# Performance work log

Hardware: AMD Instinct MI355X
Metric: run time of the kernel (lower is better)

The kernel has to match this reference:

```python
import jax, jax.numpy as jnp
import numpy as np

DIM = 512
NUM_HEADS = 8
HEAD_DIM = DIM // NUM_HEADS
MAX_SLICES = 1024
SCALE = float(np.sqrt(HEAD_DIM))


def setup_inputs() -> dict:
    key = jax.random.key(0)
    ks = jax.random.split(key, 12)
    B, Nv, Nt, D = 4, 1024, 512, DIM
    std = 0.02
    inp = {
        "visual_tokens": jax.random.normal(ks[0], (B, Nv, D), jnp.float32),
        "text_tokens": jax.random.normal(ks[1], (B, Nt, D), jnp.float32),
        # Linear weights stored as [in, out] (i.e., torch W^T), so y = x @ W + b
        "W_Q": jax.random.normal(ks[2], (D, D), jnp.float32) * std,
        "b_Q": jnp.zeros((D,), jnp.float32),
        "W_K": jax.random.normal(ks[3], (D, D), jnp.float32) * std,
        "b_K": jnp.zeros((D,), jnp.float32),
        "W_V": jax.random.normal(ks[4], (D, D), jnp.float32) * std,
        "b_V": jnp.zeros((D,), jnp.float32),
        "W_O": jax.random.normal(ks[5], (D, D), jnp.float32) * std,
        "b_O": jnp.zeros((D,), jnp.float32),
        "bias_table": jax.random.normal(ks[6], (2 * MAX_SLICES - 1, NUM_HEADS), jnp.float32) * std,
        "ln_gamma": jnp.ones((D,), jnp.float32),
        "ln_beta": jnp.zeros((D,), jnp.float32),
    }
    return inp


def _layernorm(x, gamma, beta, eps=1e-5):
    mu = jnp.mean(x, axis=-1, keepdims=True)
    var = jnp.var(x, axis=-1, keepdims=True)
    return (x - mu) * jax.lax.rsqrt(var + eps) * gamma + beta


def reference(visual_tokens, text_tokens, W_Q, b_Q, W_K, b_K, W_V, b_V, W_O, b_O,
              bias_table, ln_gamma, ln_beta):
    Z = jnp.concatenate([visual_tokens, text_tokens], axis=1)  # [B, N, D]
    B, N, D = Z.shape
    Z = _layernorm(Z, ln_gamma, ln_beta)

    def proj(W, b):
        return (Z @ W + b).reshape(B, N, NUM_HEADS, HEAD_DIM).transpose(0, 2, 1, 3)

    Q = proj(W_Q, b_Q)  # [B, H, N, hd]
    K = proj(W_K, b_K)
    V = proj(W_V, b_V)

    attn = jnp.einsum("bhqd,bhkd->bhqk", Q, K) / SCALE  # [B, H, N, N]

    # relative slice bias: [H, N, N]
    coords = jnp.arange(N)
    rel = coords[:, None] - coords[None, :] + (MAX_SLICES - 1)
    rel = jnp.clip(rel, 0, 2 * MAX_SLICES - 2)
    bias = bias_table[rel]                      # [N, N, H]
    bias = jnp.transpose(bias, (2, 0, 1))[None]  # [1, H, N, N]

    attn = jax.nn.softmax(attn + bias, axis=-1)
    out = jnp.einsum("bhqk,bhkd->bhqd", attn, V)  # [B, H, N, hd]
    out = out.transpose(0, 2, 1, 3).reshape(B, N, D)
    return out @ W_O + b_O
```

## Files before the change

kernel.cpp:

```cpp
#include <hip/hip_runtime.h>
#include <stdint.h>

#define NSEQ   1536
#define NBATCH 4
#define NM     (NBATCH * NSEQ)
#define DMODEL 512
#define NHEAD  8
#define HD     64
#define TBLN   2047

typedef __attribute__((ext_vector_type(4)))  float f32x4;
typedef __attribute__((ext_vector_type(16))) float f32x16;
typedef __attribute__((ext_vector_type(4)))  int   i32x4;
typedef __attribute__((ext_vector_type(2)))  unsigned u32x2;
typedef __attribute__((ext_vector_type(8)))  __bf16 bf16x8;
typedef unsigned short u16;

static_assert(sizeof(bf16x8) == 16, "bf16x8 must be 16B");

__device__ inline u16 f2bf(float f) {
  union { float f; uint32_t u; } v; v.f = f;
  uint32_t u = v.u;
  return (u16)((u + 0x7fffu + ((u >> 16) & 1u)) >> 16);
}

__device__ inline bf16x8 ld_bf8(const u16* p) {
  i32x4 v = *(const i32x4*)p;
  return __builtin_bit_cast(bf16x8, v);
}

__device__ inline f32x4 mfma16(bf16x8 a, bf16x8 b, f32x4 c) {
  return __builtin_amdgcn_mfma_f32_16x16x32_bf16(a, b, c, 0, 0, 0);
}

__device__ inline f32x16 mfma32(bf16x8 a, bf16x8 b, f32x16 c) {
  return __builtin_amdgcn_mfma_f32_32x32x16_bf16(a, b, c, 0, 0, 0);
}

__device__ inline void gload_lds16(const void* g, void* l) {
  __builtin_amdgcn_global_load_lds(
      (__attribute__((address_space(1))) void*)(g),
      (__attribute__((address_space(3))) void*)(l), 16, 0, 0);
}

__device__ inline uint32_t pkbf(float a, float b) {
  uint32_t r;
  asm("v_cvt_pk_bf16_f32 %0, %1, %2" : "=v"(r) : "v"(a), "v"(b));
  return r;
}

__device__ inline void plswap(uint32_t& a, uint32_t& b, int hi) {
#if __has_builtin(__builtin_amdgcn_permlane32_swap)
  u32x2 r = __builtin_amdgcn_permlane32_swap(a, b, false, false);
  a = r[0]; b = r[1];
#else
  const uint32_t as = (uint32_t)__shfl_xor((int)a, 32);
  const uint32_t bs = (uint32_t)__shfl_xor((int)b, 32);
  const uint32_t na = hi ? bs : a;
  const uint32_t nb = hi ? b : as;
  a = na; b = nb;
#endif
}

__device__ inline float exp2_raw(float x) {
  float r;
  asm("v_exp_f32 %0, %1" : "=v"(r) : "v"(x));
  return r;
}

__device__ inline float bfhi(uint32_t u) {
  union { uint32_t u; float f; } v; v.u = u & 0xffff0000u; return v.f;
}
__device__ inline float bflo(uint32_t u) {
  union { uint32_t u; float f; } v; v.u = u << 16; return v.f;
}

__global__ __launch_bounds__(256) void ln_kernel(
    const float* __restrict__ vis, const float* __restrict__ txt,
    const float* __restrict__ gamma, const float* __restrict__ beta,
    u16* __restrict__ zn) {
  const int lane = threadIdx.x & 63;
  const int row  = blockIdx.x * 4 + (threadIdx.x >> 6);
  const int b = row / NSEQ, n = row - b * NSEQ;
  const float* src = (n < 1024) ? (vis + ((size_t)b * 1024 + n) * DMODEL)
                                : (txt + ((size_t)b * 512 + (n - 1024)) * DMODEL);
  const float4* s4 = (const float4*)src;
  float4 x0 = s4[lane], x1 = s4[lane + 64];
  float s = x0.x + x0.y + x0.z + x0.w + x1.x + x1.y + x1.z + x1.w;
  float q = x0.x*x0.x + x0.y*x0.y + x0.z*x0.z + x0.w*x0.w
          + x1.x*x1.x + x1.y*x1.y + x1.z*x1.z + x1.w*x1.w;
  #pragma unroll
  for (int m = 1; m < 64; m <<= 1) { s += __shfl_xor(s, m); q += __shfl_xor(q, m); }
  const float mean = s * (1.0f / 512.0f);
  const float var  = q * (1.0f / 512.0f) - mean * mean;
  const float rstd = rsqrtf(var + 1e-5f);
  const float4* g4 = (const float4*)gamma;
  const float4* b4 = (const float4*)beta;
  float4 g0 = g4[lane], g1 = g4[lane + 64], p0 = b4[lane], p1 = b4[lane + 64];
  u16* dst = zn + (size_t)row * DMODEL;
  ushort4 o0, o1;
  o0.x = f2bf((x0.x - mean) * rstd * g0.x + p0.x);
  o0.y = f2bf((x0.y - mean) * rstd * g0.y + p0.y);
  o0.z = f2bf((x0.z - mean) * rstd * g0.z + p0.z);
  o0.w = f2bf((x0.w - mean) * rstd * g0.w + p0.w);
  o1.x = f2bf((x1.x - mean) * rstd * g1.x + p1.x);
  o1.y = f2bf((x1.y - mean) * rstd * g1.y + p1.y);
  o1.z = f2bf((x1.z - mean) * rstd * g1.z + p1.z);
  o1.w = f2bf((x1.w - mean) * rstd * g1.w + p1.w);
  *(ushort4*)(dst + lane * 4)        = o0;
  *(ushort4*)(dst + (lane + 64) * 4) = o1;
}

__global__ __launch_bounds__(256) void wtrans_kernel(
    const float* __restrict__ WQ, const float* __restrict__ WK,
    const float* __restrict__ WV, const float* __restrict__ WO,
    u16* __restrict__ wqkvt, u16* __restrict__ wot) {
  __shared__ float t[32][33];
  const int m = blockIdx.z;
  const float* W = (m == 0) ? WQ : (m == 1) ? WK : (m == 2) ? WV : WO;
  const int n0 = blockIdx.x * 32, k0 = blockIdx.y * 32;
  const int tx = threadIdx.x & 31, ty = threadIdx.x >> 5;
  #pragma unroll
  for (int j = 0; j < 4; ++j)
    t[ty + j * 8][tx] = W[(size_t)(k0 + ty + j * 8) * DMODEL + n0 + tx];
  __syncthreads();
  u16* out = (m < 3) ? (wqkvt + (size_t)m * DMODEL * DMODEL) : wot;
  #pragma unroll
  for (int j = 0; j < 4; ++j)
    out[(size_t)(n0 + ty + j * 8) * DMODEL + k0 + tx] = f2bf(t[tx][ty + j * 8]);
}

__global__ __launch_bounds__(256, 2) void gemm_qkv(
    const u16* __restrict__ A, const u16* __restrict__ Bt,
    const float* __restrict__ bQ, const float* __restrict__ bK, const float* __restrict__ bV,
    u16* __restrict__ Q, u16* __restrict__ Kk, u16* __restrict__ Vt) {
  __shared__ __align__(16) u16 lat[2][192 * 64];
  __shared__ __align__(16) u16 lbt[2][96 * 64];
  const int tid = threadIdx.x, lane = tid & 63, w = tid >> 6;
  const int wr = w >> 1, wc = w & 1;
  const int m0 = blockIdx.y * 192, n0 = blockIdx.x * 96;
  f32x4 acc[6][3] = {};
#define QSTAGE(buf, k0)                                                        \
  do {                                                                         \
    _Pragma("unroll")                                                          \
    for (int i = 0; i < 6; ++i) {                                              \
      int ch = tid + 256 * i;                              \
      int row = ch >> 3, pc = ch & 7;                                          \
      int kk = (k0) + ((pc ^ (row & 7)) << 3);                                 \
      gload_lds16(A + (size_t)(m0 + row) * DMODEL + kk, lat[buf] + (size_t)ch * 8); \
    }                                                                          \
    _Pragma("unroll")                                                          \
    for (int i = 0; i < 3; ++i) {                                              \
      int ch = tid + 256 * i;                               \
      int row = ch >> 3, pc = ch & 7;                                          \
      int kk = (k0) + ((pc ^ (row & 7)) << 3);                                 \
      gload_lds16(Bt + (size_t)(n0 + row) * DMODEL + kk, lbt[buf] + (size_t)ch * 8); \
    }                                                                          \
  } while (0)

  QSTAGE(0, 0);
  __syncthreads();
  int cur = 0;
  for (int kt = 0; kt < 8; ++kt) {
    const int nxt = cur ^ 1;
    if (kt < 7) {
      QSTAGE(nxt, (kt + 1) * 64);
      asm volatile("s_waitcnt vmcnt(9)" ::: "memory");
    } else {
      asm volatile("s_waitcnt vmcnt(0)" ::: "memory");
    }
    __builtin_amdgcn_s_barrier();
    #pragma unroll
    for (int ks = 0; ks < 2; ++ks) {
      bf16x8 af[6], bfr[3];
      const int cc = ks * 4 + (lane >> 4);
      #pragma unroll
      for (int f = 0; f < 6; ++f) {
        int ra = wr * 96 + f * 16 + (lane & 15);
        af[f]  = ld_bf8(lat[cur] + ra * 64 + ((cc ^ (ra & 7)) << 3));
      }
      #pragma unroll
      for (int f = 0; f < 3; ++f) {
        int rb = wc * 48 + f * 16 + (lane & 15);
        bfr[f] = ld_bf8(lbt[cur] + rb * 64 + ((cc ^ (rb & 7)) << 3));
      }
      __builtin_amdgcn_s_setprio(1);
      #pragma unroll
      for (int fr = 0; fr < 6; ++fr)
        #pragma unroll
        for (int fc = 0; fc < 3; ++fc)
          acc[fr][fc] = mfma16(af[fr], bfr[fc], acc[fr][fc]);
      __builtin_amdgcn_s_setprio(0);
    }
    __builtin_amdgcn_s_barrier();
    cur = nxt;
  }
  #pragma unroll
  for (int fr = 0; fr < 6; ++fr) {
    const int mbase = m0 + wr * 96 + fr * 16 + ((lane >> 4) << 2);
    const int b = mbase / NSEQ;
    const int nseq = mbase - b * NSEQ;
    #pragma unroll
    for (int fc = 0; fc < 3; ++fc) {
      const int col = n0 + wc * 48 + fc * 16 + (lane & 15);
      const int which = col >> 9;
      const int cw = col & 511;
      const int h = cw >> 6, d = cw & 63;
      const float bias = (which == 0) ? bQ[cw] : (which == 1) ? bK[cw] : bV[cw];
      if (which < 2) {
        u16* dst = ((which == 0) ? Q : Kk) + ((size_t)(b * NHEAD + h) * NSEQ + nseq) * HD + d;
        #pragma unroll
        for (int r = 0; r < 4; ++r) dst[(size_t)r * HD] = f2bf(acc[fr][fc][r] + bias);
      } else {
        ushort4 pv;
        pv.x = f2bf(acc[fr][fc][0] + bias);
        pv.y = f2bf(acc[fr][fc][1] + bias);
        pv.z = f2bf(acc[fr][fc][2] + bias);
        pv.w = f2bf(acc[fr][fc][3] + bias);
        *(ushort4*)(Vt + ((size_t)(b * NHEAD + h) * HD + d) * NSEQ + nseq) = pv;
      }
    }
  }
#undef QSTAGE
}

__global__ __launch_bounds__(256, 2) void gemm_oproj(
    const u16* __restrict__ A, const u16* __restrict__ Bt,
    const float* __restrict__ bO, float* __restrict__ out) {
  __shared__ __align__(16) u16 lat[2][96 * 64];
  __shared__ __align__(16) u16 lbt[2][64 * 64];
  const int tid = threadIdx.x, lane = tid & 63, w = tid >> 6;
  const int wr = w >> 1, wc = w & 1;
  const int m0 = blockIdx.y * 96, n0 = blockIdx.x * 64;
  f32x4 acc[3][2] = {};
#define OSTAGE(buf, k0)                                                        \
  do {                                                                         \
    _Pragma("unroll")                                                          \
    for (int i = 0; i < 3; ++i) {                                              \
      int ch = tid + 256 * i;                               \
      int row = ch >> 3, pc = ch & 7;                                          \
      int kk = (k0) + ((pc ^ (row & 7)) << 3);                                 \
      gload_lds16(A + (size_t)(m0 + row) * DMODEL + kk, lat[buf] + (size_t)ch * 8); \
    }                                                                          \
    _Pragma("unroll")                                                          \
    for (int i = 0; i < 2; ++i) {                                              \
      int ch = tid + 256 * i;                               \
      int row = ch >> 3, pc = ch & 7;                                          \
      int kk = (k0) + ((pc ^ (row & 7)) << 3);                                 \
      gload_lds16(Bt + (size_t)(n0 + row) * DMODEL + kk, lbt[buf] + (size_t)ch * 8); \
    }                                                                          \
  } while (0)

  OSTAGE(0, 0);
  __syncthreads();
  int cur = 0;
  for (int kt = 0; kt < 8; ++kt) {
    const int nxt = cur ^ 1;
    if (kt < 7) {
      OSTAGE(nxt, (kt + 1) * 64);
      asm volatile("s_waitcnt vmcnt(5)" ::: "memory");
    } else {
      asm volatile("s_waitcnt vmcnt(0)" ::: "memory");
    }
    __builtin_amdgcn_s_barrier();
    #pragma unroll
    for (int ks = 0; ks < 2; ++ks) {
      bf16x8 af[3], bfr[2];
      const int cc = ks * 4 + (lane >> 4);
      #pragma unroll
      for (int f = 0; f < 3; ++f) {
        int ra = wr * 48 + f * 16 + (lane & 15);
        af[f]  = ld_bf8(lat[cur] + ra * 64 + ((cc ^ (ra & 7)) << 3));
      }
      #pragma unroll
      for (int f = 0; f < 2; ++f) {
        int rb = wc * 32 + f * 16 + (lane & 15);
        bfr[f] = ld_bf8(lbt[cur] + rb * 64 + ((cc ^ (rb & 7)) << 3));
      }
      __builtin_amdgcn_s_setprio(1);
      #pragma unroll
      for (int fr = 0; fr < 3; ++fr)
        #pragma unroll
        for (int fc = 0; fc < 2; ++fc)
          acc[fr][fc] = mfma16(af[fr], bfr[fc], acc[fr][fc]);
      __builtin_amdgcn_s_setprio(0);
    }
    __builtin_amdgcn_s_barrier();
    cur = nxt;
  }
  #pragma unroll
  for (int fr = 0; fr < 3; ++fr) {
    const int mbase = m0 + wr * 48 + fr * 16 + ((lane >> 4) << 2);
    #pragma unroll
    for (int fc = 0; fc < 2; ++fc) {
      const int col = n0 + wc * 32 + fc * 16 + (lane & 15);
      const float bias = bO[col];
      float* dst = out + (size_t)mbase * DMODEL + col;
      #pragma unroll
      for (int r = 0; r < 4; ++r) dst[(size_t)r * DMODEL] = acc[fr][fc][r] + bias;
    }
  }
#undef OSTAGE
}

__global__ __launch_bounds__(768, 3) void attn_kernel(
    const u16* __restrict__ Q, const u16* __restrict__ K,
    const u16* __restrict__ Vt, const float* __restrict__ table,
    u16* __restrict__ O) {
  __shared__ __align__(16) char smem[77824];
  u16* rb2k = (u16*)smem;
  const int tid = threadIdx.x, lane = tid & 63, w = tid >> 6;
  const int bid = blockIdx.x;
  const int xcd = bid & 7, idx = bid >> 3;
  const int bh  = xcd * 4 + (idx & 3);
  const int qt  = idx >> 2;
  const int h   = bh & (NHEAD - 1);
  for (int t = tid; t < 2 * 3072; t += 768) {
    const int c = (t >= 3072) ? 1 : 0;
    const int x = t - c * 3072;
    int src = 2558 - (x + c);
    src = src < 0 ? 0 : (src > 2046 ? 2046 : src);
    rb2k[c * 3072 + x] = f2bf(table[(size_t)src * NHEAD + h] * 1.4426950408889634f);
  }

  const int lo32 = lane & 31, hi = lane >> 5;
  const int ws = (w < 6) ? w : (w - 6);
  const int hf = (w < 6) ? 0 : 1;
  const int kbase = hf * 768;
  const int q  = qt * 192 + ws * 32 + lo32;
  const u16* Qb = Q  + (size_t)bh * NSEQ * HD;
  const u16* Kb = K  + (size_t)bh * NSEQ * HD;
  const u16* Vb = Vt + (size_t)bh * HD * NSEQ;

  const int tloc = tid - hf * 384;
  u16* kl0 = (u16*)(smem + 12288) + hf * 2 * 4096;
  u16* vl0 = (u16*)(smem + 45056) + hf * 2 * 4096;
#define STAGE(b, k0loc)                                                       \
  if (tloc < 256) {                                                           \
    _Pragma("unroll")                                                         \
    for (int i = 0; i < 2; ++i) {                                             \
      int ch = tloc + 256 * i;                                                \
      int row = ch >> 3, pc = ch & 7;                                         \
      int col = (pc ^ (row & 7)) << 3;                                        \
      gload_lds16(Kb + (size_t)(kbase + (k0loc) + row) * HD + col,            \
                  kl0 + (size_t)(b) * 4096 + ch * 8);                         \
      gload_lds16(Vb + (size_t)row * NSEQ + kbase + (k0loc) + col,            \
                  vl0 + (size_t)(b) * 4096 + ch * 8);                         \
    }                                                                         \
  }

  bf16x8 qf[4];
  #pragma unroll
  for (int ds = 0; ds < 4; ++ds)
    qf[ds] = ld_bf8(Qb + (size_t)q * HD + ds * 16 + hi * 8);

  float l_part = 0.f;
  f32x16 acc[2] = {};

  const int rswz = lo32 & 7;
  const int T0  = 1535 - q + 4 * hi + kbase;
  const int c2  = T0 & 1;
  const int dwb = (T0 - c2) >> 1;
  const uint32_t* rbp32 = (const uint32_t*)(rb2k + c2 * 3072);
  const float c1 = 0.125f * 1.4426950408889634f;

  STAGE(0, 0);
  __syncthreads();
  int cur = 0;

  for (int kt = 0; kt < 12; ++kt) {
    const int nxt = cur ^ 1;
    if (kt < 11) {
      STAGE(nxt, (kt + 1) * 64);
      asm volatile("s_waitcnt vmcnt(4)" ::: "memory");
    } else {
      asm volatile("s_waitcnt vmcnt(0)" ::: "memory");
    }
    __builtin_amdgcn_s_barrier();
    const u16* kb = (u16*)(smem + 12288) + (hf * 2 + cur) * 4096;
    const u16* vb = (u16*)(smem + 45056) + (hf * 2 + cur) * 4096;
    #pragma unroll
    for (int ktile = 0; ktile < 2; ++ktile) {
      f32x16 st = {};
      __builtin_amdgcn_s_setprio(1);
      #pragma unroll
      for (int ds = 0; ds < 4; ++ds) {
        const int row = ktile * 32 + lo32;
        const bf16x8 kf = ld_bf8(kb + row * 64 + (((2 * ds + hi) ^ rswz) << 3));
        st = mfma32(kf, qf[ds], st);
      }
      __builtin_amdgcn_s_setprio(0);
      const int dwk = dwb + ((kt * 64 + ktile * 32) >> 1);
      float bv[4][4];
      #pragma unroll
      for (int gp = 0; gp < 4; ++gp) {
        const uint32_t u0 = rbp32[dwk + 4 * gp];
        const uint32_t u1 = rbp32[dwk + 4 * gp + 1];
        bv[gp][0] = bflo(u0); bv[gp][1] = bfhi(u0);
        bv[gp][2] = bflo(u1); bv[gp][3] = bfhi(u1);
      }
      #pragma unroll
      for (int r = 0; r < 16; ++r) {
        float p = exp2_raw(__builtin_fmaf(st[r], c1, bv[r >> 2][r & 3]));
        st[r] = p;
        l_part += p;
      }
      uint32_t wv[8];
      #pragma unroll
      for (int i = 0; i < 8; ++i) wv[i] = pkbf(st[2 * i], st[2 * i + 1]);
      plswap(wv[0], wv[2], hi);  plswap(wv[1], wv[3], hi);
      plswap(wv[4], wv[6], hi);  plswap(wv[5], wv[7], hi);
      i32x4 b0; b0[0] = (int)wv[0]; b0[1] = (int)wv[1]; b0[2] = (int)wv[2]; b0[3] = (int)wv[3];
      i32x4 b1; b1[0] = (int)wv[4]; b1[1] = (int)wv[5]; b1[2] = (int)wv[6]; b1[3] = (int)wv[7];
      const bf16x8 pb0 = __builtin_bit_cast(bf16x8, b0);
      const bf16x8 pb1 = __builtin_bit_cast(bf16x8, b1);
      __builtin_amdgcn_s_setprio(1);
      #pragma unroll
      for (int dh = 0; dh < 2; ++dh) {
        const int vrow = dh * 32 + lo32;
        const bf16x8 va0 = ld_bf8(vb + vrow * 64 + (((4 * ktile + 0 + hi) ^ rswz) << 3));
        acc[dh] = mfma32(va0, pb0, acc[dh]);
        const bf16x8 va1 = ld_bf8(vb + vrow * 64 + (((4 * ktile + 2 + hi) ^ rswz) << 3));
        acc[dh] = mfma32(va1, pb1, acc[dh]);
      }
      __builtin_amdgcn_s_setprio(0);
    }
    __builtin_amdgcn_s_barrier();
    cur = nxt;
  }
  float* scr = (float*)(smem + 12288);
  if (hf == 1) {
    float* wb = scr + ws * 2112;
    #pragma unroll
    for (int dh = 0; dh < 2; ++dh)
      #pragma unroll
      for (int i = 0; i < 4; ++i) {
        f32x4 c4; c4[0] = acc[dh][4*i]; c4[1] = acc[dh][4*i+1];
        c4[2] = acc[dh][4*i+2]; c4[3] = acc[dh][4*i+3];
        ((f32x4*)wb)[(dh * 4 + i) * 64 + lane] = c4;
      }
    wb[2048 + lane] = l_part;
  }
  __syncthreads();
  if (hf == 0) {
    const float* rb = scr + ws * 2112;
    #pragma unroll
    for (int dh = 0; dh < 2; ++dh)
      #pragma unroll
      for (int i = 0; i < 4; ++i) {
        const f32x4 c4 = ((const f32x4*)rb)[(dh * 4 + i) * 64 + lane];
        acc[dh][4*i] += c4[0]; acc[dh][4*i+1] += c4[1];
        acc[dh][4*i+2] += c4[2]; acc[dh][4*i+3] += c4[3];
      }
    l_part += rb[2048 + lane];
    float l_r = l_part + __shfl_xor(l_part, 32);
    const float inv = 1.0f / l_r;
    const int b = bh >> 3;
    u16* orow = O + ((size_t)(b * NSEQ + q)) * DMODEL + h * HD;
    #pragma unroll
    for (int dh = 0; dh < 2; ++dh)
      #pragma unroll
      for (int gp = 0; gp < 4; ++gp) {
        uint2 o4;
        o4.x = pkbf(acc[dh][4*gp]   * inv, acc[dh][4*gp+1] * inv);
        o4.y = pkbf(acc[dh][4*gp+2] * inv, acc[dh][4*gp+3] * inv);
        *(uint2*)(orow + dh * 32 + 8 * gp + 4 * hi) = o4;
      }
  }
#undef STAGE
}

extern "C" void kernel_launch(void* const* d_in, const int* in_sizes, int n_in,
                              void* d_out, int out_size, void* d_ws, size_t ws_size,
                              hipStream_t stream) {
  const float* vis   = (const float*)d_in[0];
  const float* txt   = (const float*)d_in[1];
  const float* WQ    = (const float*)d_in[2];
  const float* bQ    = (const float*)d_in[3];
  const float* WK    = (const float*)d_in[4];
  const float* bK    = (const float*)d_in[5];
  const float* WV    = (const float*)d_in[6];
  const float* bV    = (const float*)d_in[7];
  const float* WO    = (const float*)d_in[8];
  const float* bO    = (const float*)d_in[9];
  const float* table = (const float*)d_in[10];
  const float* gamma = (const float*)d_in[11];
  const float* beta  = (const float*)d_in[12];
  float* out = (float*)d_out;

  char* p = (char*)d_ws;
  u16* zn    = (u16*)p; p += (size_t)NM * DMODEL * 2;
  u16* wqkvt = (u16*)p; p += (size_t)3 * DMODEL * DMODEL * 2;
  u16* wot   = (u16*)p; p += (size_t)DMODEL * DMODEL * 2;
  u16* q     = (u16*)p; p += (size_t)NM * DMODEL * 2;
  u16* k     = (u16*)p; p += (size_t)NM * DMODEL * 2;
  u16* vt    = (u16*)p; p += (size_t)NM * DMODEL * 2;
  u16* o     = (u16*)p; p += (size_t)NM * DMODEL * 2;

  hipLaunchKernelGGL(ln_kernel, dim3(NM / 4), dim3(256), 0, stream,
                     vis, txt, gamma, beta, zn);
  hipLaunchKernelGGL(wtrans_kernel, dim3(16, 16, 4), dim3(256), 0, stream,
                     WQ, WK, WV, WO, wqkvt, wot);
  hipLaunchKernelGGL(gemm_qkv, dim3(16, 32), dim3(256), 0, stream,
                     zn, wqkvt, bQ, bK, bV, q, k, vt);
  hipLaunchKernelGGL(attn_kernel, dim3(256), dim3(768), 0, stream,
                     q, k, vt, table, o);
  hipLaunchKernelGGL(gemm_oproj, dim3(8, 64), dim3(256), 0, stream,
                     o, wot, bO, out);
}
```

Baseline: 75.44 us.

## Deepen attention K/V staging to 4-buffer ring and fuse prep kernels

The attention kernel now keeps four K/V LDS buffers and prefetches two tiles ahead, which lets it drop the trailing per-iteration barrier. The layernorm and weight-transpose kernels are merged into one launch that dispatches on block index. The aim is to hide global-load latency in attention and save one kernel launch. In exchange, attention LDS use roughly doubles and the vmcnt wait counts may not match the deeper prefetch.

```diff
diff --git a/kernel.cpp b/kernel.cpp
--- a/kernel.cpp
+++ b/kernel.cpp
@@ -75,59 +75,60 @@
   union { uint32_t u; float f; } v; v.u = u << 16; return v.f;
 }
 
-__global__ __launch_bounds__(256) void ln_kernel(
+__global__ __launch_bounds__(256) void prep_kernel(
     const float* __restrict__ vis, const float* __restrict__ txt,
     const float* __restrict__ gamma, const float* __restrict__ beta,
-    u16* __restrict__ zn) {
-  const int lane = threadIdx.x & 63;
-  const int row  = blockIdx.x * 4 + (threadIdx.x >> 6);
-  const int b = row / NSEQ, n = row - b * NSEQ;
-  const float* src = (n < 1024) ? (vis + ((size_t)b * 1024 + n) * DMODEL)
-                                : (txt + ((size_t)b * 512 + (n - 1024)) * DMODEL);
-  const float4* s4 = (const float4*)src;
-  float4 x0 = s4[lane], x1 = s4[lane + 64];
-  float s = x0.x + x0.y + x0.z + x0.w + x1.x + x1.y + x1.z + x1.w;
-  float q = x0.x*x0.x + x0.y*x0.y + x0.z*x0.z + x0.w*x0.w
-          + x1.x*x1.x + x1.y*x1.y + x1.z*x1.z + x1.w*x1.w;
-  #pragma unroll
-  for (int m = 1; m < 64; m <<= 1) { s += __shfl_xor(s, m); q += __shfl_xor(q, m); }
-  const float mean = s * (1.0f / 512.0f);
-  const float var  = q * (1.0f / 512.0f) - mean * mean;
-  const float rstd = rsqrtf(var + 1e-5f);
-  const float4* g4 = (const float4*)gamma;
-  const float4* b4 = (const float4*)beta;
-  float4 g0 = g4[lane], g1 = g4[lane + 64], p0 = b4[lane], p1 = b4[lane + 64];
-  u16* dst = zn + (size_t)row * DMODEL;
-  ushort4 o0, o1;
-  o0.x = f2bf((x0.x - mean) * rstd * g0.x + p0.x);
-  o0.y = f2bf((x0.y - mean) * rstd * g0.y + p0.y);
-  o0.z = f2bf((x0.z - mean) * rstd * g0.z + p0.z);
-  o0.w = f2bf((x0.w - mean) * rstd * g0.w + p0.w);
-  o1.x = f2bf((x1.x - mean) * rstd * g1.x + p1.x);
-  o1.y = f2bf((x1.y - mean) * rstd * g1.y + p1.y);
-  o1.z = f2bf((x1.z - mean) * rstd * g1.z + p1.z);
-  o1.w = f2bf((x1.w - mean) * rstd * g1.w + p1.w);
-  *(ushort4*)(dst + lane * 4)        = o0;
-  *(ushort4*)(dst + (lane + 64) * 4) = o1;
-}
-
-__global__ __launch_bounds__(256) void wtrans_kernel(
     const float* __restrict__ WQ, const float* __restrict__ WK,
     const float* __restrict__ WV, const float* __restrict__ WO,
-    u16* __restrict__ wqkvt, u16* __restrict__ wot) {
+    u16* __restrict__ zn, u16* __restrict__ wqkvt, u16* __restrict__ wot) {
   __shared__ float t[32][33];
-  const int m = blockIdx.z;
-  const float* W = (m == 0) ? WQ : (m == 1) ? WK : (m == 2) ? WV : WO;
-  const int n0 = blockIdx.x * 32, k0 = blockIdx.y * 32;
-  const int tx = threadIdx.x & 31, ty = threadIdx.x >> 5;
-  #pragma unroll
-  for (int j = 0; j < 4; ++j)
-    t[ty + j * 8][tx] = W[(size_t)(k0 + ty + j * 8) * DMODEL + n0 + tx];
-  __syncthreads();
-  u16* out = (m < 3) ? (wqkvt + (size_t)m * DMODEL * DMODEL) : wot;
-  #pragma unroll
-  for (int j = 0; j < 4; ++j)
-    out[(size_t)(n0 + ty + j * 8) * DMODEL + k0 + tx] = f2bf(t[tx][ty + j * 8]);
+  if (blockIdx.x < 1536) {
+    const int lane = threadIdx.x & 63;
+    const int row  = blockIdx.x * 4 + (threadIdx.x >> 6);
+    const int b = row / NSEQ, n = row - b * NSEQ;
+    const float* src = (n < 1024) ? (vis + ((size_t)b * 1024 + n) * DMODEL)
+                                  : (txt + ((size_t)b * 512 + (n - 1024)) * DMODEL);
+    const float4* s4 = (const float4*)src;
+    float4 x0 = s4[lane], x1 = s4[lane + 64];
+    float s = x0.x + x0.y + x0.z + x0.w + x1.x + x1.y + x1.z + x1.w;
+    float q = x0.x*x0.x + x0.y*x0.y + x0.z*x0.z + x0.w*x0.w
+            + x1.x*x1.x + x1.y*x1.y + x1.z*x1.z + x1.w*x1.w;
+    #pragma unroll
+    for (int m = 1; m < 64; m <<= 1) { s += __shfl_xor(s, m); q += __shfl_xor(q, m); }
+    const float mean = s * (1.0f / 512.0f);
+    const float var  = q * (1.0f / 512.0f) - mean * mean;
+    const float rstd = rsqrtf(var + 1e-5f);
+    const float4* g4 = (const float4*)gamma;
+    const float4* b4 = (const float4*)beta;
+    float4 g0 = g4[lane], g1 = g4[lane + 64], p0 = b4[lane], p1 = b4[lane + 64];
+    u16* dst = zn + (size_t)row * DMODEL;
+    ushort4 o0, o1;
+    o0.x = f2bf((x0.x - mean) * rstd * g0.x + p0.x);
+    o0.y = f2bf((x0.y - mean) * rstd * g0.y + p0.y);
+    o0.z = f2bf((x0.z - mean) * rstd * g0.z + p0.z);
+    o0.w = f2bf((x0.w - mean) * rstd * g0.w + p0.w);
+    o1.x = f2bf((x1.x - mean) * rstd * g1.x + p1.x);
+    o1.y = f2bf((x1.y - mean) * rstd * g1.y + p1.y);
+    o1.z = f2bf((x1.z - mean) * rstd * g1.z + p1.z);
+    o1.w = f2bf((x1.w - mean) * rstd * g1.w + p1.w);
+    *(ushort4*)(dst + lane * 4)        = o0;
+    *(ushort4*)(dst + (lane + 64) * 4) = o1;
+  } else {
+    const int id = blockIdx.x - 1536;
+    const int m = id & 3;
+    const int rem = id >> 2;
+    const float* W = (m == 0) ? WQ : (m == 1) ? WK : (m == 2) ? WV : WO;
+    const int n0 = (rem & 15) * 32, k0 = (rem >> 4) * 32;
+    const int tx = threadIdx.x & 31, ty = threadIdx.x >> 5;
+    #pragma unroll
+    for (int j = 0; j < 4; ++j)
+      t[ty + j * 8][tx] = W[(size_t)(k0 + ty + j * 8) * DMODEL + n0 + tx];
+    __syncthreads();
+    u16* out = (m < 3) ? (wqkvt + (size_t)m * DMODEL * DMODEL) : wot;
+    #pragma unroll
+    for (int j = 0; j < 4; ++j)
+      out[(size_t)(n0 + ty + j * 8) * DMODEL + k0 + tx] = f2bf(t[tx][ty + j * 8]);
+  }
 }
 
 __global__ __launch_bounds__(256, 2) void gemm_qkv(
@@ -144,14 +145,14 @@
   do {                                                                         \
     _Pragma("unroll")                                                          \
     for (int i = 0; i < 6; ++i) {                                              \
-      int ch = tid + 256 * i;                              \
+      int ch = tid + 256 * i;                                                  \
       int row = ch >> 3, pc = ch & 7;                                          \
       int kk = (k0) + ((pc ^ (row & 7)) << 3);                                 \
       gload_lds16(A + (size_t)(m0 + row) * DMODEL + kk, lat[buf] + (size_t)ch * 8); \
     }                                                                          \
     _Pragma("unroll")                                                          \
     for (int i = 0; i < 3; ++i) {                                              \
-      int ch = tid + 256 * i;                               \
+      int ch = tid + 256 * i;                                                  \
       int row = ch >> 3, pc = ch & 7;                                          \
       int kk = (k0) + ((pc ^ (row & 7)) << 3);                                 \
       gload_lds16(Bt + (size_t)(n0 + row) * DMODEL + kk, lbt[buf] + (size_t)ch * 8); \
@@ -237,14 +238,14 @@
   do {                                                                         \
     _Pragma("unroll")                                                          \
     for (int i = 0; i < 3; ++i) {                                              \
-      int ch = tid + 256 * i;                               \
+      int ch = tid + 256 * i;                                                  \
       int row = ch >> 3, pc = ch & 7;                                          \
       int kk = (k0) + ((pc ^ (row & 7)) << 3);                                 \
       gload_lds16(A + (size_t)(m0 + row) * DMODEL + kk, lat[buf] + (size_t)ch * 8); \
     }                                                                          \
     _Pragma("unroll")                                                          \
     for (int i = 0; i < 2; ++i) {                                              \
-      int ch = tid + 256 * i;                               \
+      int ch = tid + 256 * i;                                                  \
       int row = ch >> 3, pc = ch & 7;                                          \
       int kk = (k0) + ((pc ^ (row & 7)) << 3);                                 \
       gload_lds16(Bt + (size_t)(n0 + row) * DMODEL + kk, lbt[buf] + (size_t)ch * 8); \
@@ -307,7 +308,7 @@
     const u16* __restrict__ Q, const u16* __restrict__ K,
     const u16* __restrict__ Vt, const float* __restrict__ table,
     u16* __restrict__ O) {
-  __shared__ __align__(16) char smem[77824];
+  __shared__ __align__(16) char smem[143360];
   u16* rb2k = (u16*)smem;
   const int tid = threadIdx.x, lane = tid & 63, w = tid >> 6;
   const int bid = blockIdx.x;
@@ -333,8 +334,8 @@
   const u16* Vb = Vt + (size_t)bh * HD * NSEQ;
 
   const int tloc = tid - hf * 384;
-  u16* kl0 = (u16*)(smem + 12288) + hf * 2 * 4096;
-  u16* vl0 = (u16*)(smem + 45056) + hf * 2 * 4096;
+  u16* kl0 = (u16*)(smem + 12288) + hf * 4 * 4096;
+  u16* vl0 = (u16*)(smem + 77824) + hf * 4 * 4096;
 #define STAGE(b, k0loc)                                                       \
   if (tloc < 256) {                                                           \
     _Pragma("unroll")                                                         \
@@ -365,20 +366,19 @@
   const float c1 = 0.125f * 1.4426950408889634f;
 
   STAGE(0, 0);
+  STAGE(1, 64);
   __syncthreads();
-  int cur = 0;
 
   for (int kt = 0; kt < 12; ++kt) {
-    const int nxt = cur ^ 1;
-    if (kt < 11) {
-      STAGE(nxt, (kt + 1) * 64);
+    if (kt <= 9) {
+      STAGE((kt + 2) & 3, (kt + 2) * 64);
       asm volatile("s_waitcnt vmcnt(4)" ::: "memory");
     } else {
       asm volatile("s_waitcnt vmcnt(0)" ::: "memory");
     }
     __builtin_amdgcn_s_barrier();
-    const u16* kb = (u16*)(smem + 12288) + (hf * 2 + cur) * 4096;
-    const u16* vb = (u16*)(smem + 45056) + (hf * 2 + cur) * 4096;
+    const u16* kb = kl0 + (kt & 3) * 4096;
+    const u16* vb = vl0 + (kt & 3) * 4096;
     #pragma unroll
     for (int ktile = 0; ktile < 2; ++ktile) {
       f32x16 st = {};
@@ -425,10 +425,9 @@
       }
       __builtin_amdgcn_s_setprio(0);
     }
-    __builtin_amdgcn_s_barrier();
-    cur = nxt;
   }
   float* scr = (float*)(smem + 12288);
+  __syncthreads();
   if (hf == 1) {
     float* wb = scr + ws * 2112;
     #pragma unroll
@@ -497,10 +496,8 @@
   u16* vt    = (u16*)p; p += (size_t)NM * DMODEL * 2;
   u16* o     = (u16*)p; p += (size_t)NM * DMODEL * 2;
 
-  hipLaunchKernelGGL(ln_kernel, dim3(NM / 4), dim3(256), 0, stream,
-                     vis, txt, gamma, beta, zn);
-  hipLaunchKernelGGL(wtrans_kernel, dim3(16, 16, 4), dim3(256), 0, stream,
-                     WQ, WK, WV, WO, wqkvt, wot);
+  hipLaunchKernelGGL(prep_kernel, dim3(2560), dim3(256), 0, stream,
+                     vis, txt, gamma, beta, WQ, WK, WV, WO, zn, wqkvt, wot);
   hipLaunchKernelGGL(gemm_qkv, dim3(16, 32), dim3(256), 0, stream,
                      zn, wqkvt, bQ, bK, bV, q, k, vt);
   hipLaunchKernelGGL(attn_kernel, dim3(256), dim3(768), 0, stream,
```

Result: faster. 72.55 us (median of 2 runs) (-3.8%).
